# Kernel optimization log

Measured on AMD Instinct MI355X. Metric: run time of the kernel, lower is better.

Reference implementation:

```python
import jax, jax.numpy as jnp
import numpy as np

N_SAMPLES = 32768


def fft_shift(a, shift):
    n = a.shape[-1]
    shift_samples = shift * (n / 3.0)  # trailing dim of shift is 1 -> broadcasts over coeffs
    pad = [(0, 0)] * (a.ndim - 1) + [(0, 2 * n)]
    spec = jnp.fft.rfft(jnp.pad(a, pad), axis=-1, norm='ortho')
    n_coeffs = spec.shape[-1]
    phase = jnp.arange(n_coeffs) * (2j * jnp.pi / n_coeffs)
    spec = spec * jnp.exp(-phase * shift_samples)
    out = jnp.fft.irfft(spec, n=3 * n, axis=-1, norm='ortho')
    return out[..., :n]


def interp_linear(x, out_size):
    # matches torch F.interpolate(mode='linear', align_corners=False)
    in_size = x.shape[-1]
    scale = in_size / out_size
    coords = (jnp.arange(out_size, dtype=x.dtype) + 0.5) * scale - 0.5
    coords = jnp.clip(coords, 0.0, in_size - 1)
    i0 = jnp.floor(coords).astype(jnp.int32)
    i1 = jnp.minimum(i0 + 1, in_size - 1)
    w = coords - i0.astype(x.dtype)
    return x[..., i0] * (1.0 - w) + x[..., i1] * w


def instrument(t, shift, energy, properties):
    batch, n_events, time_len = t.shape
    t = fft_shift(t, shift)  # (b,e,T)
    _, _, cp, n_frames = energy.shape
    frame_shifts = jnp.linspace(0.0, 1.0, n_frames)
    # (b,e,1,T) shifted per-frame -> (b,e,F,T)
    exp_t = fft_shift(t[:, :, None, :], frame_shifts[None, None, :, None])
    exp_t = exp_t[:, :, None, :, :]  # (b,e,1,F,T)
    # triu mask with offset 2: mask[i,j]=1 iff j >= i+2
    mask = (jnp.arange(time_len)[None, :] >= (jnp.arange(n_frames)[:, None] + 2)).astype(t.dtype)
    mask = fft_shift(mask[None, None], shift[:, :, None, :])  # (b,e,F,T)
    mass = properties[..., :1, None]      # (b,e,cp,1,1)
    friction = properties[..., 1:, None]  # (b,e,cp,1,1)
    x = energy[..., None] * jnp.exp(-friction / (2.0 * mass) * exp_t)  # (b,e,cp,F,T)
    x = x * mask[:, :, None, :, :]
    return jnp.sum(x, axis=-2)  # (b,e,cp,T)


def reference(time, shifts, energy, shape, properties, w_pos, b_pos, w_layers, b_layers):
    batch, n_events, cp, n_frames = energy.shape
    channels, enc = w_pos.shape
    # positional filterbank -> embed -> (1,1,channels,N)
    freqs = jnp.linspace(1e-05, 0.5, enc)
    tt = jnp.linspace(0.0, float(N_SAMPLES), N_SAMPLES)
    p = jnp.sin(tt[:, None] * freqs[None, :] * jnp.pi)  # (N, enc)
    pos = (p @ w_pos.T + b_pos).T[None, None]  # (1,1,channels,N)
    # envelopes
    env = instrument(time, shifts, energy, properties)  # (b,e,cp,T)
    env = jax.nn.relu(interp_linear(env, N_SAMPLES))    # (b,e,cp,N)
    # shape network (residual layers use only l2: x + l2(relu(x)))
    s = jnp.swapaxes(shape, -1, -2)  # (b,e,F,channels)
    for i in range(w_layers.shape[0]):
        s = s + jax.nn.relu(s) @ w_layers[i].T + b_layers[i]
    s = jax.nn.relu(s)
    s = jnp.swapaxes(s, -1, -2)           # (b,e,channels,F)
    s = interp_linear(s, N_SAMPLES)       # (b,e,channels,N)
    x = pos * s * env                      # cp == channels
    return jnp.sum(x, axis=2)              # (b,e,N)


def setup_inputs():
    key = jax.random.key(0)
    ks = jax.random.split(key, 9)
    B, E, CP, F_, T, CH, ENC, L = 2, 8, 32, 64, 2048, 32, 256, 4
    return {
        'time': jax.random.uniform(ks[0], (B, E, T), dtype=jnp.float32),
        'shifts': jax.random.uniform(ks[1], (B, E, 1), dtype=jnp.float32),
        'energy': jax.random.uniform(ks[2], (B, E, CP, F_), dtype=jnp.float32),
        'shape': jax.random.normal(ks[3], (B, E, CH, F_), dtype=jnp.float32),
        'properties': jax.random.uniform(ks[4], (B, E, CP, 2), dtype=jnp.float32) + 0.5,
        'w_pos': jax.random.normal(ks[5], (CH, ENC), dtype=jnp.float32) * 0.06,
        'b_pos': jax.random.normal(ks[6], (CH,), dtype=jnp.float32) * 0.02,
        'w_layers': jax.random.normal(ks[7], (L, CH, CH), dtype=jnp.float32) * 0.15,
        'b_layers': jax.random.normal(ks[8], (L, CH), dtype=jnp.float32) * 0.02,
    }
```

## Files before the change

### kernel.cpp

```cpp
#include <hip/hip_runtime.h>
#include <math.h>

#define TL 2048
#define PI_D 3.14159265358979323846

typedef __attribute__((ext_vector_type(8))) short short8v;
typedef __attribute__((ext_vector_type(4))) float float4v;

#define BROW 4144
#define BSTRIDE 3168
#define A_BYTES 32768

__device__ __forceinline__ unsigned short bf16_rne(float f) {
  unsigned u = __float_as_uint(f);
  return (unsigned short)((u + 0x7FFFu + ((u >> 16) & 1u)) >> 16);
}

__device__ __forceinline__ float tap_val(int idx, double beta, double wv) {
  int d = idx - 2047;
  double x = PI_D * (double)d / 6144.0 - beta;
  if (fabs(x) < 1e-9) return 1.0f;
  double c = wv * (cos(x) / sin(x));
  if (d & 1) c = -c;
  return (float)c;
}

__global__ __launch_bounds__(256) void build_shift_k(const float* __restrict__ shifts,
                                                     const float* __restrict__ time_in,
                                                     const float* __restrict__ w_pos,
                                                     float* __restrict__ kerC,
                                                     unsigned short* __restrict__ BFrep,
                                                     unsigned short* __restrict__ tsh_b,
                                                     unsigned short* __restrict__ Whl) {
  __shared__ __align__(16) unsigned char sm1[17408];
  __shared__ float wsum[4];
  int b = blockIdx.x;
  int tid = threadIdx.x;
  if (b < 80) {
    float* kf = (float*)sm1;
    double s;
    if (b < 64) s = (double)b * (1.0 / 63.0) * (2048.0 / 3.0);
    else        s = (double)shifts[b - 64] * (2048.0 / 3.0);
    double beta = PI_D * s / 3073.0;
    double y = 3072.0 * s / 3073.0;
    double r = y - rint(y);
    double wv = -sin(2.0 * PI_D * r) / 6144.0;
    for (int idx = tid; idx < 4104; idx += 256)
      kf[idx] = (idx < 4095) ? tap_val(idx, beta, wv) : 0.0f;
    __syncthreads();
    if (b < 64) {
      int sr = tid >> 5, lane5 = tid & 31;
#pragma unroll
      for (int it = 0; it < 17; ++it) {
        int m = lane5 + (it << 5);
        if (m < 518) {
          unsigned short out[8];
#pragma unroll
          for (int i = 0; i < 8; ++i) {
            int arg = 4095 - (8 * m + i) + sr;
            out[i] = (arg >= 0) ? bf16_rne(kf[arg]) : (unsigned short)0;
          }
          *(short8v*)(BFrep + ((size_t)(b * 8 + sr)) * BROW + 8 * m) = *(short8v*)out;
        }
      }
    } else {
      float s0 = 0.f;
      int base = tid * 16;
#pragma unroll
      for (int i = 0; i < 16; ++i) s0 += kf[base + i];
      int lane = tid & 63;
      float v = s0;
#pragma unroll
      for (int d = 1; d < 64; d <<= 1) {
        float o = __shfl_up(v, (unsigned)d, 64);
        if (lane >= d) v += o;
      }
      if (lane == 63) wsum[tid >> 6] = v;
      __syncthreads();
      float woff = 0.f;
      for (int k = 0; k < (tid >> 6); ++k) woff += wsum[k];
      float run = v + woff - s0;
      float* crow = kerC + (b - 64) * 4096;
#pragma unroll
      for (int i = 0; i < 16; ++i) {
        crow[base + i] = run;
        run += kf[base + i];
      }
    }
  } else if (b < 336) {
    int idx = b - 80;
    int p = idx >> 4, tile = idx & 15;
    int t0 = tile * 128;
    float* a = (float*)sm1;
    float* kw = (float*)(sm1 + 8192);
    float* partial = (float*)(sm1 + 16896);
    double s = (double)shifts[p] * (2048.0 / 3.0);
    double beta = PI_D * s / 3073.0;
    double y = 3072.0 * s / 3073.0;
    double r = y - rint(y);
    double wv = -sin(2.0 * PI_D * r) / 6144.0;
    for (int i = tid; i < 2048; i += 256) a[i] = time_in[p * 2048 + i];
    for (int i = tid; i < 2175; i += 256) kw[i] = tap_val(t0 + i, beta, wv);
    __syncthreads();
    int tl = tid & 127, uh = tid >> 7;
    int base = tl + 2047 - (uh << 10);
    int u0 = uh << 10;
    float acc = 0.f;
#pragma unroll 8
    for (int u2 = 0; u2 < 1024; ++u2) acc = fmaf(a[u0 + u2], kw[base - u2], acc);
    __syncthreads();
    if (uh == 1) partial[tl] = acc;
    __syncthreads();
    if (uh == 0) {
      acc += partial[tl];
      tsh_b[p * 2048 + t0 + tl] = bf16_rne(acc);
    }
  } else {
    int c0 = (b - 336) * 1024 + tid * 4;
#pragma unroll
    for (int k2 = 0; k2 < 4; ++k2) {
      int c = c0 + k2;
      int sel = c & 1, g = (c >> 1) & 3, p16v = (c >> 3) & 15;
      int kc = (c >> 7) & 7, ct = c >> 10;
      const float* wrow = w_pos + (ct * 16 + p16v) * 256 + kc * 32 + g * 8;
      short8v ov;
#pragma unroll
      for (int i = 0; i < 8; ++i) {
        float vv = wrow[i];
        unsigned short hb = bf16_rne(vv);
        if (sel == 0) ov[i] = (short)hb;
        else {
          float hf = __uint_as_float(((unsigned)hb) << 16);
          ov[i] = (short)bf16_rne(vv - hf);
        }
      }
      *(short8v*)(Whl + (size_t)c * 8) = ov;
    }
  }
}

__global__ __launch_bounds__(512, 4) void fused3_k(const unsigned short* __restrict__ tsh_b,
                                                   const unsigned short* __restrict__ BFrep,
                                                   float* __restrict__ expTh,
                                                   const unsigned short* __restrict__ Whl,
                                                   const float* __restrict__ b_pos,
                                                   float* __restrict__ pos,
                                                   const float* __restrict__ shape,
                                                   const float* __restrict__ w_layers,
                                                   const float* __restrict__ b_layers,
                                                   float* __restrict__ s64) {
  __shared__ __align__(16) unsigned char smem[A_BYTES + 8 * BSTRIDE];
  int bx = blockIdx.x;
  int tid = threadIdx.x;
  if (bx < 512) {
    int j = bx & 63;
    int kh = (bx >> 6) & 1;
    int tQ = bx >> 7;
    int l = tid & 63, w = tid >> 6;
    int p16 = l & 15, g = l >> 4;
    int srep = p16 & 7, hb = p16 >> 3;
    const unsigned short* grow = BFrep + (size_t)j * 8 * BROW;
    int z_lo = 1536 - 512 * tQ + 1024 * kh;

#pragma unroll
    for (int it = 0; it < 4; ++it) {
      int c = tid + (it << 9);
      int pp = c >> 7, m = c & 127;
      short8v v = *(const short8v*)(tsh_b + pp * 2048 + kh * 1024 + (m << 3));
      int dst = ((pp << 11) + (m << 4)) ^ ((pp & 7) << 4);
      *(short8v*)(smem + dst) = v;
    }
    {
      int sr = tid >> 6, lane6 = tid & 63;
      const unsigned short* srcrow = grow + sr * BROW + z_lo;
      unsigned char* dstrow = smem + A_BYTES + sr * BSTRIDE;
#pragma unroll
      for (int it = 0; it < 4; ++it) {
        int m = lane6 + (it << 6);
        if (m < 197) {
          short8v v = *(const short8v*)(srcrow + (m << 3));
          *(short8v*)(dstrow + (m << 4)) = v;
        }
      }
    }
    __syncthreads();

    float4v acc[4];
#pragma unroll
    for (int i = 0; i < 4; ++i) acc[i] = (float4v){0.f, 0.f, 0.f, 0.f};
    int bBbase = A_BYTES + srep * BSTRIDE + 1024 - (w << 7) - (hb << 4) + (g << 4);
    short8v W2 = *(const short8v*)(smem + bBbase - 64);
    short8v W3 = *(const short8v*)(smem + bBbase - 96);
#pragma unroll 4
    for (int kc = 0; kc < 32; ++kc) {
      int ao = ((p16 << 11) + (kc << 6) + (g << 4)) ^ ((p16 & 7) << 4);
      short8v a = *(const short8v*)(smem + ao);
      int fb = bBbase + (kc << 6);
      short8v W0 = *(const short8v*)(smem + fb);
      short8v W1 = *(const short8v*)(smem + fb - 32);
      acc[0] = __builtin_amdgcn_mfma_f32_16x16x32_bf16(a, W0, acc[0], 0, 0, 0);
      acc[1] = __builtin_amdgcn_mfma_f32_16x16x32_bf16(a, W1, acc[1], 0, 0, 0);
      acc[2] = __builtin_amdgcn_mfma_f32_16x16x32_bf16(a, W2, acc[2], 0, 0, 0);
      acc[3] = __builtin_amdgcn_mfma_f32_16x16x32_bf16(a, W3, acc[3], 0, 0, 0);
      W2 = W0;
      W3 = W1;
    }
    float* dst = expTh + (size_t)kh * (16 * 64 * 2048);
    int tcb = 512 * tQ + 64 * w + p16;
#pragma unroll
    for (int ct = 0; ct < 4; ++ct) {
#pragma unroll
      for (int rr = 0; rr < 4; ++rr) {
        int prow = (g << 2) + rr;
        dst[(size_t)(prow * 64 + j) * TL + tcb + (ct << 4)] = acc[ct][rr];
      }
    }
  } else if (bx < 768) {
    int l = tid & 63, w = tid >> 6;
    int p16 = l & 15, g = l >> 4;
    int T0 = (bx - 512) * 128 + w * 16;

    float ttv = (float)(T0 + p16) * (32768.0f / 32767.0f);
    float4v acc0 = {0.f, 0.f, 0.f, 0.f};
    float4v acc1 = {0.f, 0.f, 0.f, 0.f};
    const short8v* Wt = (const short8v*)Whl;
    int fbase = (p16 << 3) + (g << 1);
#pragma unroll
    for (int kc = 0; kc < 8; ++kc) {
      short8v bh0 = Wt[(kc << 7) + fbase];
      short8v bl0 = Wt[(kc << 7) + fbase + 1];
      short8v bh1 = Wt[1024 + (kc << 7) + fbase];
      short8v bl1 = Wt[1024 + (kc << 7) + fbase + 1];
      short8v ahi, alo;
#pragma unroll
      for (int i = 0; i < 8; ++i) {
        int f = kc * 32 + g * 8 + i;
        float fr = 1e-5f + (float)f * ((0.5f - 1e-5f) / 255.0f);
        float rev = ttv * (0.5f * fr);
        float sv = __builtin_amdgcn_sinf(__builtin_amdgcn_fractf(rev));
        unsigned short hbit = bf16_rne(sv);
        float hf = __uint_as_float(((unsigned)hbit) << 16);
        ahi[i] = (short)hbit;
        alo[i] = (short)bf16_rne(sv - hf);
      }
      acc0 = __builtin_amdgcn_mfma_f32_16x16x32_bf16(ahi, bh0, acc0, 0, 0, 0);
      acc1 = __builtin_amdgcn_mfma_f32_16x16x32_bf16(ahi, bh1, acc1, 0, 0, 0);
      acc0 = __builtin_amdgcn_mfma_f32_16x16x32_bf16(ahi, bl0, acc0, 0, 0, 0);
      acc1 = __builtin_amdgcn_mfma_f32_16x16x32_bf16(ahi, bl1, acc1, 0, 0, 0);
      acc0 = __builtin_amdgcn_mfma_f32_16x16x32_bf16(alo, bh0, acc0, 0, 0, 0);
      acc1 = __builtin_amdgcn_mfma_f32_16x16x32_bf16(alo, bh1, acc1, 0, 0, 0);
    }
    float bp0 = b_pos[p16], bp1 = b_pos[16 + p16];
    float4v o0, o1;
#pragma unroll
    for (int rr = 0; rr < 4; ++rr) {
      o0[rr] = acc0[rr] + bp0;
      o1[rr] = acc1[rr] + bp1;
    }
    int Tr = T0 + g * 4;
    *(float4v*)(pos + (size_t)p16 * 32768 + Tr) = o0;
    *(float4v*)(pos + (size_t)(16 + p16) * 32768 + Tr) = o1;
  } else {
    float(*sA)[33] = (float(*)[33])(smem);
    float(*sB)[33] = (float(*)[33])(smem + 8448);
    float(*W)[33] = (float(*)[33])(smem + 16896);
    float* bb = (float*)(smem + 25344);
    int p = bx - 768;
    for (int idx = tid; idx < 2048; idx += 512) {
      int c = idx >> 6, f = idx & 63;
      sA[f][c] = shape[p * 2048 + idx];
    }
    int c = tid & 31, fg = tid >> 5;
    for (int ll = 0; ll < 4; ++ll) {
      for (int idx = tid; idx < 1024; idx += 512) W[idx >> 5][idx & 31] = w_layers[ll * 1024 + idx];
      if (tid < 32) bb[tid] = b_layers[ll * 32 + tid];
      __syncthreads();
      float(*cur)[33] = (ll & 1) ? sB : sA;
      float(*nxt)[33] = (ll & 1) ? sA : sB;
#pragma unroll
      for (int i = 0; i < 4; ++i) {
        int f = fg * 4 + i;
        float acc = cur[f][c] + bb[c];
#pragma unroll
        for (int k = 0; k < 32; ++k) acc = fmaf(fmaxf(cur[f][k], 0.f), W[c][k], acc);
        nxt[f][c] = acc;
      }
      __syncthreads();
    }
    for (int idx = tid; idx < 2048; idx += 512) {
      int cc = idx >> 6, f = idx & 63;
      s64[p * 2048 + idx] = fmaxf(sA[f][cc], 0.f);
    }
  }
}

__global__ __launch_bounds__(256) void env2_k(const float* __restrict__ energy,
                                              const float* __restrict__ props,
                                              const float* __restrict__ expTh,
                                              const float* __restrict__ kerC,
                                              float* __restrict__ env) {
  int p = blockIdx.x >> 5, tile = blockIdx.x & 31;
  int tl = threadIdx.x & 63;
  int cg = threadIdx.x >> 6;
  int tC = tile * 64;
  int t = tC + tl;
  __shared__ float Et[64][36];
  __shared__ float K[32];
  __shared__ float kcl[2112];
  for (int i = threadIdx.x; i < 2048; i += 256) Et[i & 63][i >> 6] = energy[p * 2048 + i];
  const float* crow = kerC + p * 4096;
  for (int i = threadIdx.x; i < 2110; i += 256) kcl[i] = crow[tC + i];
  if (threadIdx.x < 32) {
    float mass = props[(p * 32 + threadIdx.x) * 2];
    float fric = props[(p * 32 + threadIdx.x) * 2 + 1];
    K[threadIdx.x] = fric / (2.0f * mass);
  }
  __syncthreads();
  float acc[8];
  float kk[8];
#pragma unroll
  for (int i = 0; i < 8; ++i) acc[i] = 0.f;
#pragma unroll
  for (int i = 0; i < 8; ++i) kk[i] = K[cg * 8 + i];
  float Ct = kcl[tl];
  const float* xrow0 = expTh + (size_t)p * 64 * TL + t;
  const float* xrow1 = xrow0 + (size_t)16 * 64 * TL;
  for (int jj = 0; jj < 64; ++jj) {
    float x = xrow0[jj * TL] + xrow1[jj * TL];
    float mv = kcl[tl + 2046 - jj] - Ct;
    float4v e0 = *(const float4v*)(&Et[jj][cg * 8]);
    float4v e1 = *(const float4v*)(&Et[jj][cg * 8 + 4]);
#pragma unroll
    for (int cc = 0; cc < 4; ++cc)
      acc[cc] = fmaf(e0[cc] * mv, __expf(-kk[cc] * x), acc[cc]);
#pragma unroll
    for (int cc = 0; cc < 4; ++cc)
      acc[4 + cc] = fmaf(e1[cc] * mv, __expf(-kk[4 + cc] * x), acc[4 + cc]);
  }
#pragma unroll
  for (int cc = 0; cc < 8; ++cc)
    env[(size_t)(p * 32 + cg * 8 + cc) * TL + t] = acc[cc];
}

__global__ __launch_bounds__(256) void final_k(const float* __restrict__ pos,
                                               const float* __restrict__ s64,
                                               const float* __restrict__ env,
                                               float* __restrict__ out) {
  int gid = blockIdx.x * 256 + threadIdx.x;
  int p = gid >> 15, T = gid & 32767;
  float ft = (float)T + 0.5f;
  float ce = fminf(fmaxf(ft * 0.0625f - 0.5f, 0.f), 2047.f);
  int ie = (int)ce;
  int ie1 = min(ie + 1, 2047);
  float we = ce - (float)ie;
  float cs = fminf(fmaxf(ft * (1.0f / 512.0f) - 0.5f, 0.f), 63.f);
  int is0 = (int)cs;
  int is1 = min(is0 + 1, 63);
  float ws = cs - (float)is0;
  const float* erow = env + (size_t)p * 32 * TL;
  const float* srow = s64 + p * 32 * 64;
  float acc = 0.f;
  for (int c = 0; c < 32; ++c) {
    float pv = pos[(size_t)c * 32768 + T];
    float ev = fmaxf(erow[c * TL + ie] * (1.f - we) + erow[c * TL + ie1] * we, 0.f);
    float sv = srow[c * 64 + is0] * (1.f - ws) + srow[c * 64 + is1] * ws;
    acc += pv * sv * ev;
  }
  out[gid] = acc;
}

extern "C" void kernel_launch(void* const* d_in, const int* in_sizes, int n_in,
                              void* d_out, int out_size, void* d_ws, size_t ws_size,
                              hipStream_t stream) {
  const float* time_in  = (const float*)d_in[0];
  const float* shifts   = (const float*)d_in[1];
  const float* energy   = (const float*)d_in[2];
  const float* shape    = (const float*)d_in[3];
  const float* props    = (const float*)d_in[4];
  const float* w_pos    = (const float*)d_in[5];
  const float* b_pos    = (const float*)d_in[6];
  const float* w_layers = (const float*)d_in[7];
  const float* b_layers = (const float*)d_in[8];

  float* ws = (float*)d_ws;
  float* kerC = ws;
  unsigned short* BFrep = (unsigned short*)(ws + 65536);
  unsigned short* tsh_b = (unsigned short*)(ws + 1126400);
  float* expTh = ws + 1142784;
  float* pos  = ws + 5337088;
  float* s64  = ws + 6385664;
  unsigned short* Whl = (unsigned short*)(ws + 6418432);
  float* env  = ws + 6434816;
  float* out  = (float*)d_out;

  hipLaunchKernelGGL(build_shift_k, dim3(340), dim3(256), 0, stream,
                     shifts, time_in, w_pos, kerC, BFrep, tsh_b, Whl);
  hipLaunchKernelGGL(fused3_k, dim3(784), dim3(512), 0, stream, tsh_b, BFrep, expTh,
                     Whl, b_pos, pos, shape, w_layers, b_layers, s64);
  hipLaunchKernelGGL(env2_k, dim3(512), dim3(256), 0, stream, energy, props, expTh, kerC, env);
  hipLaunchKernelGGL(final_k, dim3(2048), dim3(256), 0, stream, pos, s64, env, out);
}
```

Baseline: 89.22 us.

## Fuse envelope computation with final interpolation-sum kernel via shared-memory halo

Merges the envelope kernel and the final output kernel into one launch. Each block keeps its 64-sample envelope tile plus two halo columns in shared memory, computing the halos redundantly with a split reduction, then performs the linear interpolation and channel sum directly. This removes the global env buffer round trip and one kernel launch. In exchange it adds redundant halo exp work, and the final stage now runs on 512 blocks with 4 outputs per thread instead of 2048 blocks.

```diff
diff --git a/kernel.cpp b/kernel.cpp
--- a/kernel.cpp
+++ b/kernel.cpp
@@ -54,13 +54,13 @@
       for (int it = 0; it < 17; ++it) {
         int m = lane5 + (it << 5);
         if (m < 518) {
-          unsigned short out[8];
+          unsigned short out8[8];
 #pragma unroll
           for (int i = 0; i < 8; ++i) {
             int arg = 4095 - (8 * m + i) + sr;
-            out[i] = (arg >= 0) ? bf16_rne(kf[arg]) : (unsigned short)0;
+            out8[i] = (arg >= 0) ? bf16_rne(kf[arg]) : (unsigned short)0;
           }
-          *(short8v*)(BFrep + ((size_t)(b * 8 + sr)) * BROW + 8 * m) = *(short8v*)out;
+          *(short8v*)(BFrep + ((size_t)(b * 8 + sr)) * BROW + 8 * m) = *(short8v*)out8;
         }
       }
     } else {
@@ -205,14 +205,14 @@
       W2 = W0;
       W3 = W1;
     }
-    float* dst = expTh + (size_t)kh * (16 * 64 * 2048);
+    float* dstp = expTh + (size_t)kh * (16 * 64 * 2048);
     int tcb = 512 * tQ + 64 * w + p16;
 #pragma unroll
     for (int ct = 0; ct < 4; ++ct) {
 #pragma unroll
       for (int rr = 0; rr < 4; ++rr) {
         int prow = (g << 2) + rr;
-        dst[(size_t)(prow * 64 + j) * TL + tcb + (ct << 4)] = acc[ct][rr];
+        dstp[(size_t)(prow * 64 + j) * TL + tcb + (ct << 4)] = acc[ct][rr];
       }
     }
   } else if (bx < 768) {
@@ -294,79 +294,110 @@
   }
 }
 
-__global__ __launch_bounds__(256) void env2_k(const float* __restrict__ energy,
-                                              const float* __restrict__ props,
-                                              const float* __restrict__ expTh,
-                                              const float* __restrict__ kerC,
-                                              float* __restrict__ env) {
-  int p = blockIdx.x >> 5, tile = blockIdx.x & 31;
-  int tl = threadIdx.x & 63;
-  int cg = threadIdx.x >> 6;
-  int tC = tile * 64;
-  int t = tC + tl;
+__global__ __launch_bounds__(256) void envfinal2_k(const float* __restrict__ energy,
+                                                   const float* __restrict__ props,
+                                                   const float* __restrict__ expTh,
+                                                   const float* __restrict__ kerC,
+                                                   const float* __restrict__ pos,
+                                                   const float* __restrict__ s64,
+                                                   float* __restrict__ out) {
   __shared__ float Et[64][36];
   __shared__ float K[32];
   __shared__ float kcl[2112];
-  for (int i = threadIdx.x; i < 2048; i += 256) Et[i & 63][i >> 6] = energy[p * 2048 + i];
+  __shared__ float env_s[32][68];
+  __shared__ float hpart[2][32][4];
+  int p = blockIdx.x >> 5, tile = blockIdx.x & 31;
+  int tid = threadIdx.x;
+  int tC = tile * 64, tCm1 = tC - 1;
+  for (int i = tid; i < 2048; i += 256) Et[i & 63][i >> 6] = energy[p * 2048 + i];
   const float* crow = kerC + p * 4096;
-  for (int i = threadIdx.x; i < 2110; i += 256) kcl[i] = crow[tC + i];
-  if (threadIdx.x < 32) {
-    float mass = props[(p * 32 + threadIdx.x) * 2];
-    float fric = props[(p * 32 + threadIdx.x) * 2 + 1];
-    K[threadIdx.x] = fric / (2.0f * mass);
+  for (int i = tid; i < 2112; i += 256) {
+    int gi = tCm1 + i;
+    kcl[i] = (gi >= 0) ? crow[gi] : 0.f;
+  }
+  if (tid < 32) {
+    float mass = props[(p * 32 + tid) * 2];
+    float fric = props[(p * 32 + tid) * 2 + 1];
+    K[tid] = fric / (2.0f * mass);
   }
   __syncthreads();
-  float acc[8];
-  float kk[8];
-#pragma unroll
-  for (int i = 0; i < 8; ++i) acc[i] = 0.f;
-#pragma unroll
-  for (int i = 0; i < 8; ++i) kk[i] = K[cg * 8 + i];
-  float Ct = kcl[tl];
-  const float* xrow0 = expTh + (size_t)p * 64 * TL + t;
-  const float* xrow1 = xrow0 + (size_t)16 * 64 * TL;
-  for (int jj = 0; jj < 64; ++jj) {
-    float x = xrow0[jj * TL] + xrow1[jj * TL];
-    float mv = kcl[tl + 2046 - jj] - Ct;
-    float4v e0 = *(const float4v*)(&Et[jj][cg * 8]);
-    float4v e1 = *(const float4v*)(&Et[jj][cg * 8 + 4]);
-#pragma unroll
-    for (int cc = 0; cc < 4; ++cc)
-      acc[cc] = fmaf(e0[cc] * mv, __expf(-kk[cc] * x), acc[cc]);
-#pragma unroll
-    for (int cc = 0; cc < 4; ++cc)
-      acc[4 + cc] = fmaf(e1[cc] * mv, __expf(-kk[4 + cc] * x), acc[4 + cc]);
-  }
-#pragma unroll
-  for (int cc = 0; cc < 8; ++cc)
-    env[(size_t)(p * 32 + cg * 8 + cc) * TL + t] = acc[cc];
-}
-
-__global__ __launch_bounds__(256) void final_k(const float* __restrict__ pos,
-                                               const float* __restrict__ s64,
-                                               const float* __restrict__ env,
-                                               float* __restrict__ out) {
-  int gid = blockIdx.x * 256 + threadIdx.x;
-  int p = gid >> 15, T = gid & 32767;
-  float ft = (float)T + 0.5f;
-  float ce = fminf(fmaxf(ft * 0.0625f - 0.5f, 0.f), 2047.f);
-  int ie = (int)ce;
-  int ie1 = min(ie + 1, 2047);
-  float we = ce - (float)ie;
-  float cs = fminf(fmaxf(ft * (1.0f / 512.0f) - 0.5f, 0.f), 63.f);
-  int is0 = (int)cs;
-  int is1 = min(is0 + 1, 63);
-  float ws = cs - (float)is0;
-  const float* erow = env + (size_t)p * 32 * TL;
-  const float* srow = s64 + p * 32 * 64;
-  float acc = 0.f;
-  for (int c = 0; c < 32; ++c) {
-    float pv = pos[(size_t)c * 32768 + T];
-    float ev = fmaxf(erow[c * TL + ie] * (1.f - we) + erow[c * TL + ie1] * we, 0.f);
-    float sv = srow[c * 64 + is0] * (1.f - ws) + srow[c * 64 + is1] * ws;
-    acc += pv * sv * ev;
-  }
-  out[gid] = acc;
+  int tl = tid & 63, cg = tid >> 6;
+  {
+    float acc[8];
+    float kk[8];
+#pragma unroll
+    for (int i = 0; i < 8; ++i) acc[i] = 0.f;
+#pragma unroll
+    for (int i = 0; i < 8; ++i) kk[i] = K[cg * 8 + i];
+    float Ct = kcl[tl + 1];
+    const float* xrow0 = expTh + (size_t)p * 64 * TL + (tC + tl);
+    const float* xrow1 = xrow0 + (size_t)16 * 64 * TL;
+    for (int jj = 0; jj < 64; ++jj) {
+      float x = xrow0[jj * TL] + xrow1[jj * TL];
+      float mv = kcl[tl + 1 + 2046 - jj] - Ct;
+      float4v e0 = *(const float4v*)(&Et[jj][cg * 8]);
+      float4v e1 = *(const float4v*)(&Et[jj][cg * 8 + 4]);
+#pragma unroll
+      for (int cc = 0; cc < 4; ++cc)
+        acc[cc] = fmaf(e0[cc] * mv, __expf(-kk[cc] * x), acc[cc]);
+#pragma unroll
+      for (int cc = 0; cc < 4; ++cc)
+        acc[4 + cc] = fmaf(e1[cc] * mv, __expf(-kk[4 + cc] * x), acc[4 + cc]);
+    }
+#pragma unroll
+    for (int cc = 0; cc < 8; ++cc) env_s[cg * 8 + cc][tl + 1] = acc[cc];
+  }
+  {
+    int hcol = tid >> 7, rest = tid & 127;
+    int c = rest >> 2, js = rest & 3;
+    int t = tCm1 + hcol * 65;
+    int tcl2 = min(max(t, 0), 2047);
+    int ttc = hcol * 65;
+    float Ct = kcl[ttc];
+    float kc_ = K[c];
+    const float* x0 = expTh + (size_t)p * 64 * TL + tcl2;
+    const float* x1 = x0 + (size_t)16 * 64 * TL;
+    float a = 0.f;
+    int j0 = js * 16;
+#pragma unroll
+    for (int jj = j0; jj < j0 + 16; ++jj) {
+      float x = x0[jj * TL] + x1[jj * TL];
+      float mv = kcl[ttc + 2046 - jj] - Ct;
+      a = fmaf(Et[jj][c] * mv, __expf(-kc_ * x), a);
+    }
+    hpart[hcol][c][js] = a;
+  }
+  __syncthreads();
+  if (tid < 64) {
+    int hcol = tid >> 5, c = tid & 31;
+    env_s[c][hcol * 65] =
+        hpart[hcol][c][0] + hpart[hcol][c][1] + hpart[hcol][c][2] + hpart[hcol][c][3];
+  }
+  __syncthreads();
+  int T0 = tile * 1024;
+  const float* srow = s64 + p * 2048;
+#pragma unroll
+  for (int q = 0; q < 4; ++q) {
+    int T = T0 + q * 256 + tid;
+    float ft = (float)T + 0.5f;
+    float ce = fminf(fmaxf(ft * 0.0625f - 0.5f, 0.f), 2047.f);
+    int ie = (int)ce;
+    int ie1 = min(ie + 1, 2047);
+    float we = ce - (float)ie;
+    int iel = ie - tCm1, iel1 = ie1 - tCm1;
+    float cs = fminf(fmaxf(ft * (1.0f / 512.0f) - 0.5f, 0.f), 63.f);
+    int is0 = (int)cs;
+    int is1 = min(is0 + 1, 63);
+    float wsv = cs - (float)is0;
+    float acc = 0.f;
+    for (int c = 0; c < 32; ++c) {
+      float pv = pos[(size_t)c * 32768 + T];
+      float ev = fmaxf(env_s[c][iel] * (1.f - we) + env_s[c][iel1] * we, 0.f);
+      float sv = srow[c * 64 + is0] * (1.f - wsv) + srow[c * 64 + is1] * wsv;
+      acc += pv * sv * ev;
+    }
+    out[(size_t)p * 32768 + T] = acc;
+  }
 }
 
 extern "C" void kernel_launch(void* const* d_in, const int* in_sizes, int n_in,
@@ -390,13 +421,12 @@
   float* pos  = ws + 5337088;
   float* s64  = ws + 6385664;
   unsigned short* Whl = (unsigned short*)(ws + 6418432);
-  float* env  = ws + 6434816;
   float* out  = (float*)d_out;
 
   hipLaunchKernelGGL(build_shift_k, dim3(340), dim3(256), 0, stream,
                      shifts, time_in, w_pos, kerC, BFrep, tsh_b, Whl);
   hipLaunchKernelGGL(fused3_k, dim3(784), dim3(512), 0, stream, tsh_b, BFrep, expTh,
                      Whl, b_pos, pos, shape, w_layers, b_layers, s64);
-  hipLaunchKernelGGL(env2_k, dim3(512), dim3(256), 0, stream, energy, props, expTh, kerC, env);
-  hipLaunchKernelGGL(final_k, dim3(2048), dim3(256), 0, stream, pos, s64, env, out);
-}
+  hipLaunchKernelGGL(envfinal2_k, dim3(512), dim3(256), 0, stream,
+                     energy, props, expTh, kerC, pos, s64, out);
+}
```

Result: slower. 106.1 us (+18.9%).

## Vectorize shifted-time convolution via reversed shifted tap copies; widen env2 blocks

Applied to the files above, without the earlier changes.

The direct convolution in build_shift_k now stores the tap window reversed, plus three copies offset by one to three elements. Each thread can then read aligned float4 vectors of taps and time samples, and it uses two accumulators instead of doing scalar LDS reads. This raises shared memory use to about 43KB per block. Separately, env2_k moves to 512 threads per block with 4 channels per thread instead of 8, halving per-thread exp work and registers while every thread still loads expTh.

```diff
diff --git a/kernel.cpp b/kernel.cpp
--- a/kernel.cpp
+++ b/kernel.cpp
@@ -10,6 +10,7 @@
 #define BROW 4144
 #define BSTRIDE 3168
 #define A_BYTES 32768
+#define RVS 2180
 
 __device__ __forceinline__ unsigned short bf16_rne(float f) {
   unsigned u = __float_as_uint(f);
@@ -32,7 +33,7 @@
                                                      unsigned short* __restrict__ BFrep,
                                                      unsigned short* __restrict__ tsh_b,
                                                      unsigned short* __restrict__ Whl) {
-  __shared__ __align__(16) unsigned char sm1[17408];
+  __shared__ __align__(16) unsigned char sm1[43600];
   __shared__ float wsum[4];
   int b = blockIdx.x;
   int tid = threadIdx.x;
@@ -54,13 +55,13 @@
       for (int it = 0; it < 17; ++it) {
         int m = lane5 + (it << 5);
         if (m < 518) {
-          unsigned short out[8];
+          unsigned short out8[8];
 #pragma unroll
           for (int i = 0; i < 8; ++i) {
             int arg = 4095 - (8 * m + i) + sr;
-            out[i] = (arg >= 0) ? bf16_rne(kf[arg]) : (unsigned short)0;
+            out8[i] = (arg >= 0) ? bf16_rne(kf[arg]) : (unsigned short)0;
           }
-          *(short8v*)(BFrep + ((size_t)(b * 8 + sr)) * BROW + 8 * m) = *(short8v*)out;
+          *(short8v*)(BFrep + ((size_t)(b * 8 + sr)) * BROW + 8 * m) = *(short8v*)out8;
         }
       }
     } else {
@@ -92,22 +93,45 @@
     int p = idx >> 4, tile = idx & 15;
     int t0 = tile * 128;
     float* a = (float*)sm1;
-    float* kw = (float*)(sm1 + 8192);
-    float* partial = (float*)(sm1 + 16896);
+    float* Rv = (float*)(sm1 + 8192);
+    float* partial = (float*)(sm1 + 43072);
     double s = (double)shifts[p] * (2048.0 / 3.0);
     double beta = PI_D * s / 3073.0;
     double y = 3072.0 * s / 3073.0;
     double r = y - rint(y);
     double wv = -sin(2.0 * PI_D * r) / 6144.0;
     for (int i = tid; i < 2048; i += 256) a[i] = time_in[p * 2048 + i];
-    for (int i = tid; i < 2175; i += 256) kw[i] = tap_val(t0 + i, beta, wv);
+    for (int i = tid; i < 2180; i += 256) {
+      int ti = t0 + 2175 - i;
+      Rv[i] = (ti >= 0 && ti < 4095) ? tap_val(ti, beta, wv) : 0.f;
+    }
+    __syncthreads();
+    for (int i = tid; i < 3 * RVS; i += 256) {
+      int s2 = 1 + i / RVS, j = i - (s2 - 1) * RVS;
+      int src = j + s2;
+      Rv[s2 * RVS + j] = (src < 2176) ? Rv[src] : 0.f;
+    }
     __syncthreads();
     int tl = tid & 127, uh = tid >> 7;
-    int base = tl + 2047 - (uh << 10);
     int u0 = uh << 10;
-    float acc = 0.f;
+    int c0 = 128 - tl + u0;
+    int srep = c0 & 3;
+    int idx0 = c0 - srep;
+    const float* Rrow = Rv + srep * RVS + idx0;
+    const float* ap = a + u0;
+    float acc0 = 0.f, acc1 = 0.f;
 #pragma unroll 8
-    for (int u2 = 0; u2 < 1024; ++u2) acc = fmaf(a[u0 + u2], kw[base - u2], acc);
+    for (int u2 = 0; u2 < 1024; u2 += 8) {
+      float4v av0 = *(const float4v*)(ap + u2);
+      float4v kv0 = *(const float4v*)(Rrow + u2);
+      float4v av1 = *(const float4v*)(ap + u2 + 4);
+      float4v kv1 = *(const float4v*)(Rrow + u2 + 4);
+#pragma unroll
+      for (int q = 0; q < 4; ++q) acc0 = fmaf(av0[q], kv0[q], acc0);
+#pragma unroll
+      for (int q = 0; q < 4; ++q) acc1 = fmaf(av1[q], kv1[q], acc1);
+    }
+    float acc = acc0 + acc1;
     __syncthreads();
     if (uh == 1) partial[tl] = acc;
     __syncthreads();
@@ -205,14 +229,14 @@
       W2 = W0;
       W3 = W1;
     }
-    float* dst = expTh + (size_t)kh * (16 * 64 * 2048);
+    float* dstp = expTh + (size_t)kh * (16 * 64 * 2048);
     int tcb = 512 * tQ + 64 * w + p16;
 #pragma unroll
     for (int ct = 0; ct < 4; ++ct) {
 #pragma unroll
       for (int rr = 0; rr < 4; ++rr) {
         int prow = (g << 2) + rr;
-        dst[(size_t)(prow * 64 + j) * TL + tcb + (ct << 4)] = acc[ct][rr];
+        dstp[(size_t)(prow * 64 + j) * TL + tcb + (ct << 4)] = acc[ct][rr];
       }
     }
   } else if (bx < 768) {
@@ -294,52 +318,49 @@
   }
 }
 
-__global__ __launch_bounds__(256) void env2_k(const float* __restrict__ energy,
+__global__ __launch_bounds__(512) void env2_k(const float* __restrict__ energy,
                                               const float* __restrict__ props,
                                               const float* __restrict__ expTh,
                                               const float* __restrict__ kerC,
                                               float* __restrict__ env) {
   int p = blockIdx.x >> 5, tile = blockIdx.x & 31;
-  int tl = threadIdx.x & 63;
-  int cg = threadIdx.x >> 6;
+  int tid = threadIdx.x;
+  int tl = tid & 63;
+  int cg = tid >> 6;
   int tC = tile * 64;
   int t = tC + tl;
   __shared__ float Et[64][36];
   __shared__ float K[32];
   __shared__ float kcl[2112];
-  for (int i = threadIdx.x; i < 2048; i += 256) Et[i & 63][i >> 6] = energy[p * 2048 + i];
+  for (int i = tid; i < 2048; i += 512) Et[i & 63][i >> 6] = energy[p * 2048 + i];
   const float* crow = kerC + p * 4096;
-  for (int i = threadIdx.x; i < 2110; i += 256) kcl[i] = crow[tC + i];
-  if (threadIdx.x < 32) {
-    float mass = props[(p * 32 + threadIdx.x) * 2];
-    float fric = props[(p * 32 + threadIdx.x) * 2 + 1];
-    K[threadIdx.x] = fric / (2.0f * mass);
+  for (int i = tid; i < 2110; i += 512) kcl[i] = crow[tC + i];
+  if (tid < 32) {
+    float mass = props[(p * 32 + tid) * 2];
+    float fric = props[(p * 32 + tid) * 2 + 1];
+    K[tid] = fric / (2.0f * mass);
   }
   __syncthreads();
-  float acc[8];
-  float kk[8];
-#pragma unroll
-  for (int i = 0; i < 8; ++i) acc[i] = 0.f;
-#pragma unroll
-  for (int i = 0; i < 8; ++i) kk[i] = K[cg * 8 + i];
+  float acc[4];
+  float kk[4];
+#pragma unroll
+  for (int i = 0; i < 4; ++i) acc[i] = 0.f;
+#pragma unroll
+  for (int i = 0; i < 4; ++i) kk[i] = K[cg * 4 + i];
   float Ct = kcl[tl];
   const float* xrow0 = expTh + (size_t)p * 64 * TL + t;
   const float* xrow1 = xrow0 + (size_t)16 * 64 * TL;
   for (int jj = 0; jj < 64; ++jj) {
     float x = xrow0[jj * TL] + xrow1[jj * TL];
     float mv = kcl[tl + 2046 - jj] - Ct;
-    float4v e0 = *(const float4v*)(&Et[jj][cg * 8]);
-    float4v e1 = *(const float4v*)(&Et[jj][cg * 8 + 4]);
+    float4v e0 = *(const float4v*)(&Et[jj][cg * 4]);
 #pragma unroll
     for (int cc = 0; cc < 4; ++cc)
       acc[cc] = fmaf(e0[cc] * mv, __expf(-kk[cc] * x), acc[cc]);
-#pragma unroll
-    for (int cc = 0; cc < 4; ++cc)
-      acc[4 + cc] = fmaf(e1[cc] * mv, __expf(-kk[4 + cc] * x), acc[4 + cc]);
   }
 #pragma unroll
-  for (int cc = 0; cc < 8; ++cc)
-    env[(size_t)(p * 32 + cg * 8 + cc) * TL + t] = acc[cc];
+  for (int cc = 0; cc < 4; ++cc)
+    env[(size_t)(p * 32 + cg * 4 + cc) * TL + t] = acc[cc];
 }
 
 __global__ __launch_bounds__(256) void final_k(const float* __restrict__ pos,
@@ -397,6 +418,6 @@
                      shifts, time_in, w_pos, kerC, BFrep, tsh_b, Whl);
   hipLaunchKernelGGL(fused3_k, dim3(784), dim3(512), 0, stream, tsh_b, BFrep, expTh,
                      Whl, b_pos, pos, shape, w_layers, b_layers, s64);
-  hipLaunchKernelGGL(env2_k, dim3(512), dim3(256), 0, stream, energy, props, expTh, kerC, env);
+  hipLaunchKernelGGL(env2_k, dim3(512), dim3(512), 0, stream, energy, props, expTh, kerC, env);
   hipLaunchKernelGGL(final_k, dim3(2048), dim3(256), 0, stream, pos, s64, env, out);
 }
```

Measured after the change: 86.19 us. 3.4% less time.
